# Optimization experiments

Hardware: AMD Instinct MI355X
Metric: run time of the kernel (lower is better)

Reference implementation:

```python
import jax, jax.numpy as jnp
import numpy as np

N_NODES = 50000
N_EDGES = 800000
N_GRAPHS = 16
IN_C, HID, OUT, EDGE_D = 5, 128, 64, 3


def setup_inputs() -> dict:
    key = jax.random.key(0)
    ks = jax.random.split(key, 20)
    x = jax.random.normal(ks[0], (N_NODES, IN_C), jnp.float32)
    edge_index = jax.random.randint(ks[1], (2, N_EDGES), 0, N_NODES, jnp.int32)
    edge_attr = jax.random.normal(ks[2], (N_EDGES, EDGE_D), jnp.float32)
    batch = jnp.sort(jax.random.randint(ks[3], (N_NODES,), 0, N_GRAPHS, jnp.int32))
    p = lambda k, s: jax.random.normal(k, s, jnp.float32) * 0.1
    return {
        "x": x, "edge_index": edge_index, "edge_attr": edge_attr, "batch": batch,
        "W1": p(ks[4], (IN_C, HID)), "as1": p(ks[5], (HID,)), "ad1": p(ks[6], (HID,)),
        "We1": p(ks[7], (EDGE_D, HID)), "ae1": p(ks[8], (HID,)), "b1": p(ks[9], (HID,)),
        "W2": p(ks[10], (HID, OUT)), "as2": p(ks[11], (OUT,)), "ad2": p(ks[12], (OUT,)),
        "We2": p(ks[13], (EDGE_D, OUT)), "ae2": p(ks[14], (OUT,)), "b2": p(ks[15], (OUT,)),
    }


def _gat_layer(x, src, dst, edge_attr, W, a_s, a_d, We, ae, b):
    # PyG GATConv (heads=1): linear, self-loops with mean-filled edge_attr,
    # leaky-relu attention logits, softmax over destination, scatter-sum.
    N = x.shape[0]
    h = x @ W                                        # [N, C]
    ones = jnp.ones((src.shape[0],), h.dtype)
    cnt = jax.ops.segment_sum(ones, dst, num_segments=N)
    loop_attr = jax.ops.segment_sum(edge_attr, dst, num_segments=N) / jnp.maximum(cnt, 1.0)[:, None]
    idx = jnp.arange(N, dtype=src.dtype)
    s = jnp.concatenate([src, idx])                  # [E+N]
    d = jnp.concatenate([dst, idx])
    ea = jnp.concatenate([edge_attr, loop_attr], axis=0)
    alpha_s = h @ a_s                                # [N]
    alpha_d = h @ a_d
    alpha_e = (ea @ We) @ ae                         # [E+N]
    logit = jax.nn.leaky_relu(alpha_s[s] + alpha_d[d] + alpha_e, 0.2)
    m = jax.ops.segment_max(logit, d, num_segments=N)
    ex = jnp.exp(logit - m[d])
    den = jax.ops.segment_sum(ex, d, num_segments=N)
    coef = ex / den[d]                               # softmax over incoming edges
    out = jax.ops.segment_sum(coef[:, None] * h[s], d, num_segments=N)
    return out + b


def reference(x, edge_index, edge_attr, batch, W1, as1, ad1, We1, ae1, b1,
              W2, as2, ad2, We2, ae2, b2):
    src, dst = edge_index[0], edge_index[1]
    h = _gat_layer(x, src, dst, edge_attr, W1, as1, ad1, We1, ae1, b1)
    h = jax.nn.relu(h)
    h = _gat_layer(h, src, dst, edge_attr, W2, as2, ad2, We2, ae2, b2)
    # global mean pool over graphs
    tot = jax.ops.segment_sum(h, batch, num_segments=N_GRAPHS)
    cnt = jax.ops.segment_sum(jnp.ones((h.shape[0],), h.dtype), batch, num_segments=N_GRAPHS)
    return tot / jnp.maximum(cnt, 1.0)[:, None]
```

## Files before the change

### kernel.cpp

```cpp
#include <hip/hip_runtime.h>
#include <math.h>

#define N_NODESC 50000
#define N_EDGESC 800000
#define N_GRAPHSC 16
#define IN_CC 5
#define HIDC 128
#define OUTCC 64
#define SLOT 64
#define WSCALE 8388608.0f
#define WINV (1.0f / 8388608.0f)

#define NPB 128
#define NBKT ((N_NODESC + NPB - 1) / NPB)
#define EBKT 2560
#define SBLK 256
#define EPB (N_EDGESC / SBLK)

#define DW_WAS1 0
#define DW_WAD1 5
#define DW_WEAE1 10
#define DW_WEAE2 13
#define DW_WAS2 16
#define DW_WAD2 144
#define DW_TOTAL 272

__device__ __forceinline__ float leakyf(float x) { return x >= 0.0f ? x : 0.2f * x; }

__device__ __forceinline__ void fatomic(float* p, float v) {
#if defined(__AMDGCN__)
    unsafeAtomicAdd(p, v);
#else
    atomicAdd(p, v);
#endif
}

__device__ __forceinline__ unsigned int bfpack(float a, float b) {
    unsigned int ua = __float_as_uint(a), ub = __float_as_uint(b);
    ua += 0x7FFFu + ((ua >> 16) & 1u);
    ub += 0x7FFFu + ((ub >> 16) & 1u);
    return (ua & 0xFFFF0000u) | (ub >> 16);
}
__device__ __forceinline__ float bfhi(unsigned int u) { return __uint_as_float(u & 0xFFFF0000u); }
__device__ __forceinline__ float bflo(unsigned int u) { return __uint_as_float(u << 16); }

__global__ void k_derived(const float* __restrict__ W1, const float* __restrict__ as1,
                          const float* __restrict__ ad1, const float* __restrict__ We1,
                          const float* __restrict__ ae1, const float* __restrict__ W2,
                          const float* __restrict__ as2, const float* __restrict__ ad2,
                          const float* __restrict__ We2, const float* __restrict__ ae2,
                          float* __restrict__ dw, int* __restrict__ gcur) {
    for (int t = threadIdx.x; t < NBKT; t += blockDim.x) gcur[t] = 0;
    for (int t = threadIdx.x; t < DW_TOTAL; t += blockDim.x) {
        float acc = 0.0f;
        if (t < 5) {
            for (int c = 0; c < HIDC; ++c) acc += W1[t * HIDC + c] * as1[c];
        } else if (t < 10) {
            int k = t - 5;
            for (int c = 0; c < HIDC; ++c) acc += W1[k * HIDC + c] * ad1[c];
        } else if (t < 13) {
            int j = t - 10;
            for (int c = 0; c < HIDC; ++c) acc += We1[j * HIDC + c] * ae1[c];
        } else if (t < 16) {
            int j = t - 13;
            for (int c = 0; c < OUTCC; ++c) acc += We2[j * OUTCC + c] * ae2[c];
        } else if (t < 144) {
            int k = t - 16;
            for (int c = 0; c < OUTCC; ++c) acc += W2[k * OUTCC + c] * as2[c];
        } else {
            int k = t - 144;
            for (int c = 0; c < OUTCC; ++c) acc += W2[k * OUTCC + c] * ad2[c];
        }
        dw[t] = acc;
    }
}

__global__ void k_alpha1(const float* __restrict__ x, const float* __restrict__ dw,
                         float* __restrict__ xp, int4* __restrict__ wi4) {
    int n = blockIdx.x * blockDim.x + threadIdx.x;
    if (n >= N_NODESC) return;
    float a = 0.0f, b = 0.0f;
    float xv[IN_CC];
#pragma unroll
    for (int k = 0; k < IN_CC; ++k) {
        xv[k] = x[n * IN_CC + k];
        a += xv[k] * dw[DW_WAS1 + k];
        b += xv[k] * dw[DW_WAD1 + k];
    }
    *(float4*)&xp[(size_t)n * 8] = make_float4(xv[0], xv[1], xv[2], xv[3]);
    *(float4*)&xp[(size_t)n * 8 + 4] = make_float4(xv[4], a, b, 0.0f);
    int4 z = make_int4(0, 0, 0, 0);
    size_t wb = (size_t)n * 4;
    wi4[wb + 0] = z;
    wi4[wb + 1] = z;
    wi4[wb + 2] = z;
    wi4[wb + 3] = z;
}

__global__ void kC(const int* __restrict__ ei, const float* __restrict__ eattr,
                   const float* __restrict__ dw, int* __restrict__ gcur,
                   uint2* __restrict__ ebuf) {
    __shared__ int hist[NBKT];
    __shared__ int cur[NBKT];
    int blk = blockIdx.x, tid = threadIdx.x;
    for (int b = tid; b < NBKT; b += 256) hist[b] = 0;
    __syncthreads();
    int e0 = blk * EPB;
    for (int e = e0 + tid; e < e0 + EPB; e += 256)
        atomicAdd(&hist[ei[N_EDGESC + e] / NPB], 1);
    __syncthreads();
    for (int b = tid; b < NBKT; b += 256) {
        int h = hist[b];
        cur[b] = (h > 0) ? (b * EBKT + atomicAdd(&gcur[b], h)) : 0;
    }
    __syncthreads();
    float w10 = dw[DW_WEAE1 + 0], w11 = dw[DW_WEAE1 + 1], w12 = dw[DW_WEAE1 + 2];
    float w20 = dw[DW_WEAE2 + 0], w21 = dw[DW_WEAE2 + 1], w22 = dw[DW_WEAE2 + 2];
    for (int e = e0 + tid; e < e0 + EPB; e += 256) {
        int d = ei[N_EDGESC + e];
        int s = ei[e];
        int b = d / NPB;
        float a0 = eattr[e * 3 + 0], a1 = eattr[e * 3 + 1], a2 = eattr[e * 3 + 2];
        float e1v = a0 * w10 + a1 * w11 + a2 * w12;
        float e2v = a0 * w20 + a1 * w21 + a2 * w22;
        int pos = atomicAdd(&cur[b], 1);
        if (pos < (b + 1) * EBKT)
            ebuf[pos] = make_uint2((unsigned int)s | ((unsigned int)(d - b * NPB) << 16),
                                   bfpack(e1v, e2v));
    }
}

__global__ void kD(const uint2* __restrict__ ebuf, const int* __restrict__ gcur,
                   unsigned long long* __restrict__ edges, int* __restrict__ cnt) {
    __shared__ int c2[NPB];
    int b = blockIdx.x, tid = threadIdx.x;
    for (int i = tid; i < NPB; i += 256) c2[i] = 0;
    __syncthreads();
    int ne = min(gcur[b], EBKT);
    int base = b * EBKT;
    for (int i = tid; i < ne; i += 256) {
        uint2 r = ebuf[base + i];
        int dl = (r.x >> 16) & 0xFF;
        unsigned int s = r.x & 0xFFFFu;
        int rr = atomicAdd(&c2[dl], 1);
        if (rr < SLOT)
            edges[((size_t)(b * NPB + dl) << 6) + rr] =
                (unsigned long long)s | ((unsigned long long)r.y << 32);
    }
    __syncthreads();
    for (int dl = tid; dl < NPB; dl += 256) {
        int n = b * NPB + dl;
        if (n < N_NODESC) cnt[n] = min(c2[dl], SLOT);
    }
}

__global__ void k_agg1(const float* __restrict__ xp, const unsigned long long* __restrict__ edges,
                       const int* __restrict__ cnt, const float* __restrict__ W1,
                       const float* __restrict__ b1, const float* __restrict__ dw,
                       float* __restrict__ agg1p, float2* __restrict__ av2) {
    int t = blockIdx.x * blockDim.x + threadIdx.x;
    int n = t >> 4;
    int q = threadIdx.x & 15;
    if (n >= N_NODESC) return;
    int deg = cnt[n];
    size_t base = (size_t)n << 6;
    float4 sxa = *(const float4*)&xp[(size_t)n * 8];
    float4 sxb = *(const float4*)&xp[(size_t)n * 8 + 4];
    float ad = sxb.z;
    float den = 0.0f, se = 0.0f;
    float acc[IN_CC] = {0.0f, 0.0f, 0.0f, 0.0f, 0.0f};
    for (int i = q; i < deg; i += 16) {
        unsigned long long r = edges[base + i];
        int s = (int)(unsigned int)(r & 0xFFFFFFFFull);
        unsigned int ep = (unsigned int)(r >> 32);
        float e1 = bfhi(ep);
        float4 xa = *(const float4*)&xp[(size_t)s * 8];
        float4 xb = *(const float4*)&xp[(size_t)s * 8 + 4];
        float ex = __expf(leakyf(xb.y + ad + e1));
        den += ex;
        se += e1;
        acc[0] += ex * xa.x;
        acc[1] += ex * xa.y;
        acc[2] += ex * xa.z;
        acc[3] += ex * xa.w;
        acc[4] += ex * xb.x;
    }
#pragma unroll
    for (int d2 = 8; d2; d2 >>= 1) {
        den += __shfl_xor(den, d2);
        se += __shfl_xor(se, d2);
        acc[0] += __shfl_xor(acc[0], d2);
        acc[1] += __shfl_xor(acc[1], d2);
        acc[2] += __shfl_xor(acc[2], d2);
        acc[3] += __shfl_xor(acc[3], d2);
        acc[4] += __shfl_xor(acc[4], d2);
    }
    float la = se / fmaxf((float)deg, 1.0f);
    float es = __expf(leakyf(sxb.y + ad + la));
    den += es;
    float inv = 1.0f / den;
    float av[IN_CC];
    av[0] = (acc[0] + es * sxa.x) * inv;
    av[1] = (acc[1] + es * sxa.y) * inv;
    av[2] = (acc[2] + es * sxa.z) * inv;
    av[3] = (acc[3] + es * sxa.w) * inv;
    av[4] = (acc[4] + es * sxb.x) * inv;
    if (q == 0) {
        *(float4*)&agg1p[(size_t)n * 8] = make_float4(av[0], av[1], av[2], av[3]);
        agg1p[(size_t)n * 8 + 4] = av[4];
    }
    int c0 = q * 8;
    float o[8];
    {
        float4 bb0 = *(const float4*)&b1[c0];
        float4 bb1 = *(const float4*)&b1[c0 + 4];
        o[0] = bb0.x; o[1] = bb0.y; o[2] = bb0.z; o[3] = bb0.w;
        o[4] = bb1.x; o[5] = bb1.y; o[6] = bb1.z; o[7] = bb1.w;
    }
#pragma unroll
    for (int k = 0; k < IN_CC; ++k) {
        float4 w0 = *(const float4*)&W1[k * HIDC + c0];
        float4 w1 = *(const float4*)&W1[k * HIDC + c0 + 4];
        o[0] += av[k] * w0.x; o[1] += av[k] * w0.y; o[2] += av[k] * w0.z; o[3] += av[k] * w0.w;
        o[4] += av[k] * w1.x; o[5] += av[k] * w1.y; o[6] += av[k] * w1.z; o[7] += av[k] * w1.w;
    }
#pragma unroll
    for (int j = 0; j < 8; ++j) o[j] = fmaxf(o[j], 0.0f);
    float4 da0 = *(const float4*)&dw[DW_WAS2 + c0];
    float4 da1 = *(const float4*)&dw[DW_WAS2 + c0 + 4];
    float4 db0 = *(const float4*)&dw[DW_WAD2 + c0];
    float4 db1 = *(const float4*)&dw[DW_WAD2 + c0 + 4];
    float a = o[0] * da0.x + o[1] * da0.y + o[2] * da0.z + o[3] * da0.w +
              o[4] * da1.x + o[5] * da1.y + o[6] * da1.z + o[7] * da1.w;
    float b = o[0] * db0.x + o[1] * db0.y + o[2] * db0.z + o[3] * db0.w +
              o[4] * db1.x + o[5] * db1.y + o[6] * db1.z + o[7] * db1.w;
#pragma unroll
    for (int d2 = 8; d2; d2 >>= 1) {
        a += __shfl_xor(a, d2);
        b += __shfl_xor(b, d2);
    }
    if (q == 0) av2[n] = make_float2(a, b);
}

__global__ void kL2(const float2* __restrict__ av2, const unsigned long long* __restrict__ edges,
                    const int* __restrict__ cnt, const int* __restrict__ batch,
                    int* __restrict__ wi) {
    int t = blockIdx.x * blockDim.x + threadIdx.x;
    int n = t >> 4;
    int q = threadIdx.x & 15;
    if (n >= N_NODESC) return;
    int deg = cnt[n];
    size_t base = (size_t)n << 6;
    float2 an = av2[n];
    float ad = an.y;
    int g = batch[n];
    float den = 0.0f, se = 0.0f;
    float exc[4];
    int sc[4];
#pragma unroll
    for (int it = 0; it < 4; ++it) {
        exc[it] = 0.0f;
        sc[it] = 0;
        int i = q + it * 16;
        if (i < deg) {
            unsigned long long r = edges[base + i];
            int s = (int)(unsigned int)(r & 0xFFFFFFFFull);
            float e2 = bflo((unsigned int)(r >> 32));
            float ex = __expf(leakyf(av2[s].x + ad + e2));
            exc[it] = ex;
            sc[it] = s;
            den += ex;
            se += e2;
        }
    }
#pragma unroll
    for (int d2 = 8; d2; d2 >>= 1) {
        den += __shfl_xor(den, d2);
        se += __shfl_xor(se, d2);
    }
    float la = se / fmaxf((float)deg, 1.0f);
    float lself = leakyf(an.x + ad + la);
    den += __expf(lself);
    float inv = WSCALE / den;
#pragma unroll
    for (int it = 0; it < 4; ++it) {
        int i = q + it * 16;
        if (i < deg)
            atomicAdd(&wi[(size_t)sc[it] * N_GRAPHSC + g], __float2int_rn(exc[it] * inv));
    }
    if (q == 0) atomicAdd(&wi[(size_t)n * N_GRAPHSC + g], __float2int_rn(__expf(lself) * inv));
}

#define WS_PART 1024
#define WS_CHUNK ((N_NODESC + WS_PART - 1) / WS_PART)
__global__ void kWsum(const float* __restrict__ agg1p, const int* __restrict__ wi,
                      const float* __restrict__ W1, const float* __restrict__ b1,
                      float* __restrict__ part) {
    __shared__ float red[N_GRAPHSC][HIDC];
    int c = threadIdx.x & 127;
    int sub = threadIdx.x >> 7;
    float w1c[IN_CC];
#pragma unroll
    for (int k = 0; k < IN_CC; ++k) w1c[k] = W1[k * HIDC + c];
    float bb = b1[c];
    float acc[N_GRAPHSC];
#pragma unroll
    for (int g = 0; g < N_GRAPHSC; ++g) acc[g] = 0.0f;
    int start = blockIdx.x * WS_CHUNK;
    int end = min(start + WS_CHUNK, N_NODESC);
    for (int n = start + sub; n < end; n += 2) {
        float4 a4 = *(const float4*)&agg1p[(size_t)n * 8];
        float a5 = agg1p[(size_t)n * 8 + 4];
        float x2c = bb + a4.x * w1c[0] + a4.y * w1c[1] + a4.z * w1c[2] + a4.w * w1c[3] +
                    a5 * w1c[4];
        x2c = fmaxf(x2c, 0.0f) * WINV;
        const int4* wr = (const int4*)&wi[(size_t)n * N_GRAPHSC];
        int4 w0 = wr[0], w1_ = wr[1], w2_ = wr[2], w3_ = wr[3];
        acc[0] += (float)w0.x * x2c;  acc[1] += (float)w0.y * x2c;
        acc[2] += (float)w0.z * x2c;  acc[3] += (float)w0.w * x2c;
        acc[4] += (float)w1_.x * x2c; acc[5] += (float)w1_.y * x2c;
        acc[6] += (float)w1_.z * x2c; acc[7] += (float)w1_.w * x2c;
        acc[8] += (float)w2_.x * x2c; acc[9] += (float)w2_.y * x2c;
        acc[10] += (float)w2_.z * x2c; acc[11] += (float)w2_.w * x2c;
        acc[12] += (float)w3_.x * x2c; acc[13] += (float)w3_.y * x2c;
        acc[14] += (float)w3_.z * x2c; acc[15] += (float)w3_.w * x2c;
    }
    if (sub) {
#pragma unroll
        for (int g = 0; g < N_GRAPHSC; ++g) red[g][c] = acc[g];
    }
    __syncthreads();
    if (!sub) {
        float* pb = part + (size_t)blockIdx.x * (N_GRAPHSC * HIDC);
#pragma unroll
        for (int g = 0; g < N_GRAPHSC; ++g) pb[g * HIDC + c] = acc[g] + red[g][c];
    }
}

__global__ void kWreduce(const float* __restrict__ part, float* __restrict__ psum) {
    __shared__ float red[8][32];
    int col = blockIdx.x * 32 + (threadIdx.x & 31);
    int rg = threadIdx.x >> 5;
    float acc = 0.0f;
    for (int r = rg * 128; r < (rg + 1) * 128; ++r)
        acc += part[(size_t)r * (N_GRAPHSC * HIDC) + col];
    red[rg][threadIdx.x & 31] = acc;
    __syncthreads();
    if (rg == 0) {
        float s = red[0][threadIdx.x & 31];
#pragma unroll
        for (int j = 1; j < 8; ++j) s += red[j][threadIdx.x & 31];
        psum[col] = s;
    }
}

__global__ void k_final(const float* __restrict__ psum, const int* __restrict__ batch,
                        const float* __restrict__ W2, const float* __restrict__ b2,
                        float* __restrict__ out) {
    int t = blockIdx.x * blockDim.x + threadIdx.x;
    if (t >= N_GRAPHSC * OUTCC) return;
    int g = t >> 6, c = t & 63;
    int lo = 0, hi = N_NODESC;
    while (lo < hi) {
        int mid = (lo + hi) >> 1;
        if (batch[mid] < g) lo = mid + 1; else hi = mid;
    }
    int start = lo;
    lo = 0; hi = N_NODESC;
    while (lo < hi) {
        int mid = (lo + hi) >> 1;
        if (batch[mid] <= g) lo = mid + 1; else hi = mid;
    }
    float invc = 1.0f / fmaxf((float)(lo - start), 1.0f);
    float acc = 0.0f;
#pragma unroll 8
    for (int k = 0; k < HIDC; ++k) acc += psum[g * HIDC + k] * W2[k * OUTCC + c];
    out[t] = acc * invc + b2[c];
}

extern "C" void kernel_launch(void* const* d_in, const int* in_sizes, int n_in,
                              void* d_out, int out_size, void* d_ws, size_t ws_size,
                              hipStream_t stream) {
    const float* x     = (const float*)d_in[0];
    const int*   ei    = (const int*)d_in[1];
    const float* eattr = (const float*)d_in[2];
    const int*   batch = (const int*)d_in[3];
    const float* W1  = (const float*)d_in[4];
    const float* as1 = (const float*)d_in[5];
    const float* ad1 = (const float*)d_in[6];
    const float* We1 = (const float*)d_in[7];
    const float* ae1 = (const float*)d_in[8];
    const float* b1  = (const float*)d_in[9];
    const float* W2  = (const float*)d_in[10];
    const float* as2 = (const float*)d_in[11];
    const float* ad2 = (const float*)d_in[12];
    const float* We2 = (const float*)d_in[13];
    const float* ae2 = (const float*)d_in[14];
    const float* b2  = (const float*)d_in[15];
    float* out = (float*)d_out;

    char* ws = (char*)d_ws;
    size_t off = 0;
    auto alloc = [&](size_t bytes) -> void* {
        void* p = ws + off;
        off = (off + bytes + 255) & ~(size_t)255;
        return p;
    };
    int*    gcur  = (int*)alloc(NBKT * 4);
    int*    wi    = (int*)alloc((size_t)N_NODESC * N_GRAPHSC * 4);
    float*  psum  = (float*)alloc((size_t)N_GRAPHSC * HIDC * 4);
    float*  dw    = (float*)alloc(DW_TOTAL * 4);
    int*    cnt   = (int*)alloc(N_NODESC * 4);
    uint2*  ebuf  = (uint2*)alloc((size_t)NBKT * EBKT * 8);
    unsigned long long* edges = (unsigned long long*)alloc((size_t)N_NODESC * SLOT * 8);
    float*  xp    = (float*)alloc((size_t)N_NODESC * 8 * 4);
    float2* av2   = (float2*)alloc((size_t)N_NODESC * 8);
    float*  agg1p = (float*)alloc((size_t)N_NODESC * 8 * 4);
    float*  part  = (float*)alloc((size_t)WS_PART * N_GRAPHSC * HIDC * 4);

    k_derived<<<1, 256, 0, stream>>>(W1, as1, ad1, We1, ae1, W2, as2, ad2, We2, ae2, dw,
                                     gcur);
    k_alpha1<<<(N_NODESC + 255) / 256, 256, 0, stream>>>(x, dw, xp, (int4*)wi);
    kC<<<SBLK, 256, 0, stream>>>(ei, eattr, dw, gcur, ebuf);
    kD<<<NBKT, 256, 0, stream>>>(ebuf, gcur, edges, cnt);
    k_agg1<<<(N_NODESC * 16 + 255) / 256, 256, 0, stream>>>(xp, edges, cnt, W1, b1, dw,
                                                            agg1p, av2);
    kL2<<<(N_NODESC * 16 + 255) / 256, 256, 0, stream>>>(av2, edges, cnt, batch, wi);
    kWsum<<<WS_PART, 256, 0, stream>>>(agg1p, wi, W1, b1, part);
    kWreduce<<<64, 256, 0, stream>>>(part, psum);
    k_final<<<4, 256, 0, stream>>>(psum, batch, W2, b2, out);
}
```

Before: 142.3 us.

## Fold derived-weight and final-projection kernels into neighbors to cut launches

```diff
diff --git a/kernel.cpp b/kernel.cpp
--- a/kernel.cpp
+++ b/kernel.cpp
@@ -17,10 +17,6 @@
 #define SBLK 256
 #define EPB (N_EDGESC / SBLK)
 
-#define DW_WAS1 0
-#define DW_WAD1 5
-#define DW_WEAE1 10
-#define DW_WEAE2 13
 #define DW_WAS2 16
 #define DW_WAD2 144
 #define DW_TOTAL 272
@@ -44,48 +40,44 @@
 __device__ __forceinline__ float bfhi(unsigned int u) { return __uint_as_float(u & 0xFFFF0000u); }
 __device__ __forceinline__ float bflo(unsigned int u) { return __uint_as_float(u << 16); }
 
-__global__ void k_derived(const float* __restrict__ W1, const float* __restrict__ as1,
-                          const float* __restrict__ ad1, const float* __restrict__ We1,
-                          const float* __restrict__ ae1, const float* __restrict__ W2,
-                          const float* __restrict__ as2, const float* __restrict__ ad2,
-                          const float* __restrict__ We2, const float* __restrict__ ae2,
-                          float* __restrict__ dw, int* __restrict__ gcur) {
-    for (int t = threadIdx.x; t < NBKT; t += blockDim.x) gcur[t] = 0;
-    for (int t = threadIdx.x; t < DW_TOTAL; t += blockDim.x) {
+__global__ void k_alpha1(const float* __restrict__ x, const float* __restrict__ W1,
+                         const float* __restrict__ as1, const float* __restrict__ ad1,
+                         const float* __restrict__ W2, const float* __restrict__ as2,
+                         const float* __restrict__ ad2, const float* __restrict__ b2,
+                         float* __restrict__ dw, float* __restrict__ out,
+                         int* __restrict__ gcur, float* __restrict__ xp,
+                         int4* __restrict__ wi4) {
+    __shared__ float was1[IN_CC], wad1[IN_CC];
+    int tid = threadIdx.x;
+    if (tid < 2 * IN_CC) {
+        int k = (tid < IN_CC) ? tid : tid - IN_CC;
+        const float* a = (tid < IN_CC) ? as1 : ad1;
         float acc = 0.0f;
-        if (t < 5) {
-            for (int c = 0; c < HIDC; ++c) acc += W1[t * HIDC + c] * as1[c];
-        } else if (t < 10) {
-            int k = t - 5;
-            for (int c = 0; c < HIDC; ++c) acc += W1[k * HIDC + c] * ad1[c];
-        } else if (t < 13) {
-            int j = t - 10;
-            for (int c = 0; c < HIDC; ++c) acc += We1[j * HIDC + c] * ae1[c];
-        } else if (t < 16) {
-            int j = t - 13;
-            for (int c = 0; c < OUTCC; ++c) acc += We2[j * OUTCC + c] * ae2[c];
-        } else if (t < 144) {
-            int k = t - 16;
-            for (int c = 0; c < OUTCC; ++c) acc += W2[k * OUTCC + c] * as2[c];
-        } else {
-            int k = t - 144;
-            for (int c = 0; c < OUTCC; ++c) acc += W2[k * OUTCC + c] * ad2[c];
+        for (int c = 0; c < HIDC; ++c) acc += W1[k * HIDC + c] * a[c];
+        if (tid < IN_CC) was1[k] = acc; else wad1[k] = acc;
+    }
+    if (blockIdx.x == 0) {
+        {
+            int idx = tid;
+            int k = idx & 127;
+            const float* a = (idx < 128) ? as2 : ad2;
+            float acc = 0.0f;
+            for (int c = 0; c < OUTCC; ++c) acc += W2[k * OUTCC + c] * a[c];
+            dw[DW_WAS2 + idx] = acc;
         }
-        dw[t] = acc;
-    }
-}
-
-__global__ void k_alpha1(const float* __restrict__ x, const float* __restrict__ dw,
-                         float* __restrict__ xp, int4* __restrict__ wi4) {
-    int n = blockIdx.x * blockDim.x + threadIdx.x;
+        for (int t2 = tid; t2 < N_GRAPHSC * OUTCC; t2 += 256) out[t2] = b2[t2 & 63];
+        for (int t2 = tid; t2 < NBKT; t2 += 256) gcur[t2] = 0;
+    }
+    __syncthreads();
+    int n = blockIdx.x * blockDim.x + tid;
     if (n >= N_NODESC) return;
     float a = 0.0f, b = 0.0f;
     float xv[IN_CC];
 #pragma unroll
     for (int k = 0; k < IN_CC; ++k) {
         xv[k] = x[n * IN_CC + k];
-        a += xv[k] * dw[DW_WAS1 + k];
-        b += xv[k] * dw[DW_WAD1 + k];
+        a += xv[k] * was1[k];
+        b += xv[k] * wad1[k];
     }
     *(float4*)&xp[(size_t)n * 8] = make_float4(xv[0], xv[1], xv[2], xv[3]);
     *(float4*)&xp[(size_t)n * 8 + 4] = make_float4(xv[4], a, b, 0.0f);
@@ -98,11 +90,22 @@
 }
 
 __global__ void kC(const int* __restrict__ ei, const float* __restrict__ eattr,
-                   const float* __restrict__ dw, int* __restrict__ gcur,
-                   uint2* __restrict__ ebuf) {
+                   const float* __restrict__ We1, const float* __restrict__ ae1,
+                   const float* __restrict__ We2, const float* __restrict__ ae2,
+                   int* __restrict__ gcur, uint2* __restrict__ ebuf) {
     __shared__ int hist[NBKT];
     __shared__ int cur[NBKT];
+    __shared__ float ew[6];
     int blk = blockIdx.x, tid = threadIdx.x;
+    if (tid < 6) {
+        float acc = 0.0f;
+        if (tid < 3) {
+            for (int c = 0; c < HIDC; ++c) acc += We1[tid * HIDC + c] * ae1[c];
+        } else {
+            for (int c = 0; c < OUTCC; ++c) acc += We2[(tid - 3) * OUTCC + c] * ae2[c];
+        }
+        ew[tid] = acc;
+    }
     for (int b = tid; b < NBKT; b += 256) hist[b] = 0;
     __syncthreads();
     int e0 = blk * EPB;
@@ -114,8 +117,8 @@
         cur[b] = (h > 0) ? (b * EBKT + atomicAdd(&gcur[b], h)) : 0;
     }
     __syncthreads();
-    float w10 = dw[DW_WEAE1 + 0], w11 = dw[DW_WEAE1 + 1], w12 = dw[DW_WEAE1 + 2];
-    float w20 = dw[DW_WEAE2 + 0], w21 = dw[DW_WEAE2 + 1], w22 = dw[DW_WEAE2 + 2];
+    float w10 = ew[0], w11 = ew[1], w12 = ew[2];
+    float w20 = ew[3], w21 = ew[4], w22 = ew[5];
     for (int e = e0 + tid; e < e0 + EPB; e += 256) {
         int d = ei[N_EDGESC + e];
         int s = ei[e];
@@ -337,45 +340,46 @@
     }
 }
 
-__global__ void kWreduce(const float* __restrict__ part, float* __restrict__ psum) {
+__global__ void kWfinal(const float* __restrict__ part, const float* __restrict__ W2,
+                        const int* __restrict__ batch, float* __restrict__ out) {
     __shared__ float red[8][32];
-    int col = blockIdx.x * 32 + (threadIdx.x & 31);
+    __shared__ float ps[32];
+    int lane = threadIdx.x & 31;
     int rg = threadIdx.x >> 5;
+    int col = blockIdx.x * 32 + lane;
     float acc = 0.0f;
     for (int r = rg * 128; r < (rg + 1) * 128; ++r)
         acc += part[(size_t)r * (N_GRAPHSC * HIDC) + col];
-    red[rg][threadIdx.x & 31] = acc;
+    red[rg][lane] = acc;
     __syncthreads();
     if (rg == 0) {
-        float s = red[0][threadIdx.x & 31];
-#pragma unroll
-        for (int j = 1; j < 8; ++j) s += red[j][threadIdx.x & 31];
-        psum[col] = s;
-    }
-}
-
-__global__ void k_final(const float* __restrict__ psum, const int* __restrict__ batch,
-                        const float* __restrict__ W2, const float* __restrict__ b2,
-                        float* __restrict__ out) {
-    int t = blockIdx.x * blockDim.x + threadIdx.x;
-    if (t >= N_GRAPHSC * OUTCC) return;
-    int g = t >> 6, c = t & 63;
-    int lo = 0, hi = N_NODESC;
-    while (lo < hi) {
-        int mid = (lo + hi) >> 1;
-        if (batch[mid] < g) lo = mid + 1; else hi = mid;
-    }
-    int start = lo;
-    lo = 0; hi = N_NODESC;
-    while (lo < hi) {
-        int mid = (lo + hi) >> 1;
-        if (batch[mid] <= g) lo = mid + 1; else hi = mid;
-    }
-    float invc = 1.0f / fmaxf((float)(lo - start), 1.0f);
-    float acc = 0.0f;
+        float s = red[0][lane];
+#pragma unroll
+        for (int j = 1; j < 8; ++j) s += red[j][lane];
+        ps[lane] = s;
+    }
+    __syncthreads();
+    if (threadIdx.x < OUTCC) {
+        int c = threadIdx.x;
+        int g = (blockIdx.x * 32) >> 7;
+        int kbase = (blockIdx.x * 32) & 127;
+        int lo = 0, hi = N_NODESC;
+        while (lo < hi) {
+            int mid = (lo + hi) >> 1;
+            if (batch[mid] < g) lo = mid + 1; else hi = mid;
+        }
+        int start = lo;
+        lo = 0; hi = N_NODESC;
+        while (lo < hi) {
+            int mid = (lo + hi) >> 1;
+            if (batch[mid] <= g) lo = mid + 1; else hi = mid;
+        }
+        float invc = 1.0f / fmaxf((float)(lo - start), 1.0f);
+        float v = 0.0f;
 #pragma unroll 8
-    for (int k = 0; k < HIDC; ++k) acc += psum[g * HIDC + k] * W2[k * OUTCC + c];
-    out[t] = acc * invc + b2[c];
+        for (int j = 0; j < 32; ++j) v += ps[j] * W2[(kbase + j) * OUTCC + c];
+        fatomic(&out[g * OUTCC + c], v * invc);
+    }
 }
 
 extern "C" void kernel_launch(void* const* d_in, const int* in_sizes, int n_in,
@@ -408,7 +412,6 @@
     };
     int*    gcur  = (int*)alloc(NBKT * 4);
     int*    wi    = (int*)alloc((size_t)N_NODESC * N_GRAPHSC * 4);
-    float*  psum  = (float*)alloc((size_t)N_GRAPHSC * HIDC * 4);
     float*  dw    = (float*)alloc(DW_TOTAL * 4);
     int*    cnt   = (int*)alloc(N_NODESC * 4);
     uint2*  ebuf  = (uint2*)alloc((size_t)NBKT * EBKT * 8);
@@ -418,15 +421,13 @@
     float*  agg1p = (float*)alloc((size_t)N_NODESC * 8 * 4);
     float*  part  = (float*)alloc((size_t)WS_PART * N_GRAPHSC * HIDC * 4);
 
-    k_derived<<<1, 256, 0, stream>>>(W1, as1, ad1, We1, ae1, W2, as2, ad2, We2, ae2, dw,
-                                     gcur);
-    k_alpha1<<<(N_NODESC + 255) / 256, 256, 0, stream>>>(x, dw, xp, (int4*)wi);
-    kC<<<SBLK, 256, 0, stream>>>(ei, eattr, dw, gcur, ebuf);
+    k_alpha1<<<(N_NODESC + 255) / 256, 256, 0, stream>>>(x, W1, as1, ad1, W2, as2, ad2,
+                                                         b2, dw, out, gcur, xp, (int4*)wi);
+    kC<<<SBLK, 256, 0, stream>>>(ei, eattr, We1, ae1, We2, ae2, gcur, ebuf);
     kD<<<NBKT, 256, 0, stream>>>(ebuf, gcur, edges, cnt);
     k_agg1<<<(N_NODESC * 16 + 255) / 256, 256, 0, stream>>>(xp, edges, cnt, W1, b1, dw,
                                                             agg1p, av2);
     kL2<<<(N_NODESC * 16 + 255) / 256, 256, 0, stream>>>(av2, edges, cnt, batch, wi);
     kWsum<<<WS_PART, 256, 0, stream>>>(agg1p, wi, W1, b1, part);
-    kWreduce<<<64, 256, 0, stream>>>(part, psum);
-    k_final<<<4, 256, 0, stream>>>(psum, batch, W2, b2, out);
-}
+    kWfinal<<<64, 256, 0, stream>>>(part, W2, batch, out);
+}
```

New measurement: 129.0 us. -9.3%, faster.
